# Optimization experiments

Hardware: AMD Instinct MI355X
Metric: run time of the kernel (lower is better)

Reference implementation:

```python
import jax, jax.numpy as jnp
import numpy as np

B, T, V, E, H, C = 64, 512, 32000, 256, 512, 4

def setup_inputs() -> dict:
    key = jax.random.key(0)
    ks = jax.random.split(key, 8)
    s = 1.0 / np.sqrt(H)  # torch LSTM default init scale
    return {
        "x": jax.random.randint(ks[0], (B, T), 0, V),
        "emb": jax.random.normal(ks[1], (V, E), jnp.float32) * 0.1,
        "W_ih": jax.random.uniform(ks[2], (4 * H, E), jnp.float32, -s, s),
        "W_hh": jax.random.uniform(ks[3], (4 * H, H), jnp.float32, -s, s),
        "b_ih": jax.random.uniform(ks[4], (4 * H,), jnp.float32, -s, s),
        "b_hh": jax.random.uniform(ks[5], (4 * H,), jnp.float32, -s, s),
        "W_fc": jax.random.uniform(ks[6], (C, H), jnp.float32, -s, s),
        "b_fc": jax.random.uniform(ks[7], (C,), jnp.float32, -s, s),
    }

def _lstm_last_hidden(e, W_ih, W_hh, b_ih, b_hh):
    # e: [B,T,E]. Precompute input-side gate preactivations for all steps.
    xg = jnp.einsum('bte,ge->tbg', e, W_ih) + (b_ih + b_hh)  # [T,B,4H]
    h0 = jnp.zeros((e.shape[0], H), e.dtype)
    c0 = jnp.zeros((e.shape[0], H), e.dtype)

    def step(carry, xt):
        h, c = carry
        g = xt + h @ W_hh.T                       # [B,4H]
        i, f, gg, o = jnp.split(g, 4, axis=-1)    # torch gate order: i,f,g,o
        i = jax.nn.sigmoid(i)
        f = jax.nn.sigmoid(f)
        gg = jnp.tanh(gg)
        o = jax.nn.sigmoid(o)
        c = f * c + i * gg
        h = o * jnp.tanh(c)
        return (h, c), None

    (hT, _), _ = jax.lax.scan(step, (h0, c0), xg)
    return hT  # last hidden == lstm_out[:, -1, :] for unidirectional LSTM

def reference(x, emb, W_ih, W_hh, b_ih, b_hh, W_fc, b_fc):
    e = emb[x]                                    # [B,T,E] embedding lookup
    hT = _lstm_last_hidden(e, W_ih, W_hh, b_ih, b_hh)
    return hT @ W_fc.T + b_fc                     # [B,C] logits
```

## Files before the change

kernel.cpp:

```cpp
#include <hip/hip_runtime.h>
#include <hip/hip_bf16.h>

#define B_  64
#define T_  512
#define E_  256
#define H_  512
#define G4_ 2048
#define C_  4

typedef __attribute__((ext_vector_type(4))) float  f32x4;
typedef __attribute__((ext_vector_type(8))) __bf16 bf16x8;
typedef __attribute__((ext_vector_type(8))) short  short8;
typedef __attribute__((ext_vector_type(4))) short  s16x4;

union V16 { f32x4 f; bf16x8 b; short8 s; };

__device__ __forceinline__ float sigmoid_(float x) { return 1.0f / (1.0f + __expf(-x)); }
__device__ __forceinline__ float tanh_(float x)    { return 1.0f - 2.0f / (__expf(2.0f * x) + 1.0f); }

__device__ __forceinline__ short f2bf(float f) {
  union { float f; unsigned u; } v; v.f = f;
  return (short)((v.u + 0x7FFFu + ((v.u >> 16) & 1u)) >> 16);
}

__device__ __forceinline__ void store_short_llc(void* p, unsigned v) {
  asm volatile("global_store_short %0, %1, off sc0 sc1" :: "v"(p), "v"(v) : "memory");
}
__device__ __forceinline__ void store_dword_llc(void* p, float v) {
  asm volatile("global_store_dword %0, %1, off sc0 sc1" :: "v"(p), "v"(v) : "memory");
}
__device__ __forceinline__ void load2_dwordx4_llc(const void* p0, const void* p1,
                                                  f32x4* a, f32x4* b) {
  asm volatile(
      "global_load_dwordx4 %0, %2, off sc0 sc1\n\t"
      "global_load_dwordx4 %1, %3, off sc0 sc1\n\t"
      "s_waitcnt vmcnt(0)"
      : "=&v"(*a), "=&v"(*b) : "v"(p0), "v"(p1) : "memory");
}

__global__ __launch_bounds__(256, 1) void wih_conv(const float* __restrict__ W,
                                                   short* __restrict__ out) {
  const int i = (blockIdx.x * 256 + threadIdx.x) * 4;
  f32x4 v = *(const f32x4*)(W + i);
  s16x4 s;
  s[0] = f2bf(v[0]); s[1] = f2bf(v[1]); s[2] = f2bf(v[2]); s[3] = f2bf(v[3]);
  *(s16x4*)(out + i) = s;
}

template<bool WBF16>
__global__ __launch_bounds__(256, 1) void xg_kernel(
    const int* __restrict__ x, const float* __restrict__ emb,
    const void* __restrict__ Wv,
    __hip_bfloat16* __restrict__ xg)
{
  const int t   = blockIdx.x;
  const int tid = threadIdx.x;
  __shared__ int s_idx[B_];
  __shared__ __hip_bfloat16 s_e[B_][E_ + 8];

  if (tid < B_) s_idx[tid] = x[tid * T_ + t];
  __syncthreads();
  {
    int b = tid >> 2, ch = tid & 3;
    const float* src = emb + (size_t)s_idx[b] * E_ + ch * 64;
    short* dst = (short*)&s_e[b][ch * 64];
#pragma unroll
    for (int i = 0; i < 16; i++) {
      f32x4 v = *(const f32x4*)(src + i * 4);
      s16x4 s;
      s[0] = f2bf(v[0]); s[1] = f2bf(v[1]); s[2] = f2bf(v[2]); s[3] = f2bf(v[3]);
      *(s16x4*)(dst + i * 4) = s;
    }
  }
  __syncthreads();

  const int wv   = tid >> 6;
  const int lane = tid & 63;
  const int ln15 = lane & 15, quad = lane >> 4;

  V16 breg[4][8];
#pragma unroll
  for (int nt = 0; nt < 4; nt++)
#pragma unroll
    for (int ks = 0; ks < 8; ks++)
      breg[nt][ks].f = *(const f32x4*)(&s_e[nt * 16 + ln15][quad * 8 + ks * 32]);

  const int gbase = wv * 512;
  const size_t base_t = (size_t)t * (G4_ * B_);
  for (int mt = 0; mt < 32; mt++) {
    const int grow = gbase + mt * 16 + ln15;
    V16 areg[8];
    if constexpr (WBF16) {
      const short* arow = (const short*)Wv + (size_t)grow * E_ + quad * 8;
#pragma unroll
      for (int ks = 0; ks < 8; ks++)
        areg[ks].f = *(const f32x4*)(arow + ks * 32);
    } else {
      const float* arow = (const float*)Wv + (size_t)grow * E_ + quad * 8;
#pragma unroll
      for (int ks = 0; ks < 8; ks++) {
        f32x4 lo = *(const f32x4*)(arow + ks * 32);
        f32x4 hi = *(const f32x4*)(arow + ks * 32 + 4);
        short8 s;
        s[0] = f2bf(lo[0]); s[1] = f2bf(lo[1]); s[2] = f2bf(lo[2]); s[3] = f2bf(lo[3]);
        s[4] = f2bf(hi[0]); s[5] = f2bf(hi[1]); s[6] = f2bf(hi[2]); s[7] = f2bf(hi[3]);
        areg[ks].s = s;
      }
    }

    f32x4 acc[4];
#pragma unroll
    for (int nt = 0; nt < 4; nt++) acc[nt] = (f32x4){0.f, 0.f, 0.f, 0.f};
#pragma unroll
    for (int ks = 0; ks < 8; ks++)
#pragma unroll
      for (int nt = 0; nt < 4; nt++)
        acc[nt] = __builtin_amdgcn_mfma_f32_16x16x32_bf16(areg[ks].b, breg[nt][ks].b, acc[nt], 0, 0, 0);

    const int dbase = mt * 16 + quad * 4;
#pragma unroll
    for (int nt = 0; nt < 4; nt++) {
      const int batch = nt * 16 + ln15;
      s16x4 sv;
#pragma unroll
      for (int r = 0; r < 4; r++) sv[r] = f2bf(acc[nt][r]);
      *(s16x4*)((short*)xg + base_t + ((size_t)wv << 15) + ((size_t)batch << 9) + dbase) = sv;
    }
  }
}

__global__ __launch_bounds__(512, 2) void lstm_kernel(
    const float* __restrict__ W_hh,
    const float* __restrict__ b_ih, const float* __restrict__ b_hh,
    const float* __restrict__ W_fc, const float* __restrict__ b_fc,
    const __hip_bfloat16* __restrict__ xg,
    unsigned int* flags, __hip_bfloat16* hbuf , float* hT,
    float* out)
{
  const int tid  = threadIdx.x;
  const int blk  = blockIdx.x;
  const int pb   = blk & 3;
  const int pd   = blk >> 2;
  const int d0   = pd * 32;
  const int wv   = tid >> 6;
  const int lane = tid & 63;
  const int ln15 = lane & 15, quad = lane >> 4;

  __shared__ __hip_bfloat16 s_h[16][520];
  __shared__ float s_pre[4][16][36];

  V16 areg[16];
  {
    const int grow = (wv >> 1) * 512 + d0 + (wv & 1) * 16 + ln15;
    const float* ap = W_hh + (size_t)grow * H_ + quad * 8;
#pragma unroll
    for (int ks = 0; ks < 16; ks++) {
      f32x4 lo = *(const f32x4*)(ap + ks * 32);
      f32x4 hi = *(const f32x4*)(ap + ks * 32 + 4);
      short8 s;
      s[0] = f2bf(lo[0]); s[1] = f2bf(lo[1]); s[2] = f2bf(lo[2]); s[3] = f2bf(lo[3]);
      s[4] = f2bf(hi[0]); s[5] = f2bf(hi[1]); s[6] = f2bf(hi[2]); s[7] = f2bf(hi[3]);
      areg[ks].s = s;
    }
  }

  const int nb = tid >> 5;
  const int nd = tid & 31;
  const int gb = pb * 16 + nb;
  const int dg = d0 + nd;
  const float bias_i = b_ih[dg]        + b_hh[dg];
  const float bias_f = b_ih[512 + dg]  + b_hh[512 + dg];
  const float bias_g = b_ih[1024 + dg] + b_hh[1024 + dg];
  const float bias_o = b_ih[1536 + dg] + b_hh[1536 + dg];
  float c = 0.0f;
  const int myflag = pb * 16 + pd;

  for (int t = 0; t < T_; t++) {
    const int cur = t & 1, nxt = cur ^ 1;

    const size_t xoff = (size_t)t * (G4_ * B_) + ((size_t)gb << 9) + dg;
    const __hip_bfloat16 xgi = xg[xoff];
    const __hip_bfloat16 xgf = xg[xoff + (1u << 15)];
    const __hip_bfloat16 xgg = xg[xoff + (2u << 15)];
    const __hip_bfloat16 xgo = xg[xoff + (3u << 15)];

    if (tid < 16) {
      const unsigned* fp = flags + pb * 16 + tid;
      while (__hip_atomic_load(fp, __ATOMIC_RELAXED, __HIP_MEMORY_SCOPE_AGENT) < (unsigned)t) {}
    }
    __syncthreads();

    {
      const short* hbase = (const short*)hbuf + (size_t)cur * (B_ * H_) + (size_t)(pb * 16) * H_;
      const int i0 = tid, i1 = tid + 512;
      f32x4 va, vb;
      load2_dwordx4_llc(hbase + i0 * 8, hbase + i1 * 8, &va, &vb);
      *(f32x4*)&s_h[i0 >> 6][(i0 & 63) * 8] = va;
      *(f32x4*)&s_h[i1 >> 6][(i1 & 63) * 8] = vb;
    }
    __syncthreads();

    f32x4 acc0 = (f32x4){0.f, 0.f, 0.f, 0.f};
    f32x4 acc1 = (f32x4){0.f, 0.f, 0.f, 0.f};
#pragma unroll
    for (int ks = 0; ks < 16; ks += 2) {
      V16 b0, b1;
      b0.f = *(const f32x4*)&s_h[ln15][quad * 8 + ks * 32];
      b1.f = *(const f32x4*)&s_h[ln15][quad * 8 + (ks + 1) * 32];
      acc0 = __builtin_amdgcn_mfma_f32_16x16x32_bf16(areg[ks].b,     b0.b, acc0, 0, 0, 0);
      acc1 = __builtin_amdgcn_mfma_f32_16x16x32_bf16(areg[ks + 1].b, b1.b, acc1, 0, 0, 0);
    }
    const f32x4 accs = acc0 + acc1;

    *(f32x4*)&s_pre[wv >> 1][ln15][(wv & 1) * 16 + quad * 4] = accs;
    __syncthreads();

    {
      const float pi = s_pre[0][nb][nd] + bias_i + __bfloat162float(xgi);
      const float pf = s_pre[1][nb][nd] + bias_f + __bfloat162float(xgf);
      const float pg = s_pre[2][nb][nd] + bias_g + __bfloat162float(xgg);
      const float po = s_pre[3][nb][nd] + bias_o + __bfloat162float(xgo);
      const float i_ = sigmoid_(pi), f_ = sigmoid_(pf);
      const float g_ = tanh_(pg),    o_ = sigmoid_(po);
      c = f_ * c + i_ * g_;
      const float h = o_ * tanh_(c);
      if (t < T_ - 1) {
        store_short_llc((short*)hbuf + (size_t)nxt * (B_ * H_) + (size_t)gb * H_ + dg,
                        (unsigned)(unsigned short)f2bf(h));
      } else {
        store_dword_llc(hT + gb * H_ + dg, h);
      }
    }
    __syncthreads();

    if (tid == 0)
      __hip_atomic_store(&flags[myflag], (unsigned)(t + 1),
                         __ATOMIC_RELAXED, __HIP_MEMORY_SCOPE_AGENT);
  }

  if (blk == 0) {
    if (tid < 64)
      while (__hip_atomic_load(&flags[tid], __ATOMIC_RELAXED, __HIP_MEMORY_SCOPE_AGENT) < (unsigned)T_) {}
    __builtin_amdgcn_fence(__ATOMIC_ACQUIRE, "agent");
    __syncthreads();
    for (int o = tid; o < B_ * C_; o += 512) {
      const int b = o >> 2, cl = o & 3;
      const f32x4* hr = (const f32x4*)(hT + b * H_);
      const f32x4* wr = (const f32x4*)(W_fc + cl * H_);
      float s = 0.f;
      for (int d4 = 0; d4 < H_ / 4; d4++) {
        const f32x4 hv = hr[d4];
        const f32x4 wv4 = wr[d4];
        s += hv[0] * wv4[0] + hv[1] * wv4[1] + hv[2] * wv4[2] + hv[3] * wv4[3];
      }
      s += b_fc[cl];
      out[o] = s;
    }
  }
}

extern "C" void kernel_launch(void* const* d_in, const int* in_sizes, int n_in,
                              void* d_out, int out_size, void* d_ws, size_t ws_size,
                              hipStream_t stream) {
  const int*   x    = (const int*)d_in[0];
  const float* emb  = (const float*)d_in[1];
  const float* W_ih = (const float*)d_in[2];
  const float* W_hh = (const float*)d_in[3];
  const float* b_ih = (const float*)d_in[4];
  const float* b_hh = (const float*)d_in[5];
  const float* W_fc = (const float*)d_in[6];
  const float* b_fc = (const float*)d_in[7];
  float* out = (float*)d_out;

  char* ws = (char*)d_ws;
  const size_t XG_OFF  = 524288;
  const size_t XG_END  = XG_OFF + (size_t)T_ * G4_ * B_ * 2;
  const size_t NEEDED2 = XG_END + (size_t)G4_ * E_ * 2;
  if (ws_size < XG_END) return;

  unsigned int*   flags = (unsigned int*)ws;
  __hip_bfloat16* hbuf  = (__hip_bfloat16*)(ws + 4096);
  float*          hT    = (float*)(ws + 135168);
  __hip_bfloat16* xg    = (__hip_bfloat16*)(ws + XG_OFF);
  short*          wih16 = (short*)(ws + XG_END);

  (void)hipMemsetAsync(ws, 0, 135168, stream);

  if (ws_size >= NEEDED2) {
    wih_conv<<<512, 256, 0, stream>>>(W_ih, wih16);
    xg_kernel<true><<<T_, 256, 0, stream>>>(x, emb, wih16, xg);
  } else {
    xg_kernel<false><<<T_, 256, 0, stream>>>(x, emb, W_ih, xg);
  }
  lstm_kernel<<<64, 512, 0, stream>>>(W_hh, b_ih, b_hh, W_fc, b_fc, xg,
                                      flags, hbuf, hT, out);
}
```

Measured before the change: 1.343 ms.

## Repartition LSTM blocks into 8 batch groups by 64 hidden units

The recurrent kernel's 64 blocks are regrouped from 4 batch groups × 32 hidden units into 8 batch groups × 64 hidden units. Each block now waits on only 8 producer flags and reads half as much of h per step, which shrinks the cross-block dependency fan-in. The price is that each wave holds two W_hh tiles and runs two MFMA chains of 16. Because only 8 batches are live, half of each 16-wide MFMA tile is zero padding. That doubles per-step MFMA work and register pressure.

```diff
diff --git a/kernel.cpp b/kernel.cpp
--- a/kernel.cpp
+++ b/kernel.cpp
@@ -29,13 +29,11 @@
 __device__ __forceinline__ void store_dword_llc(void* p, float v) {
   asm volatile("global_store_dword %0, %1, off sc0 sc1" :: "v"(p), "v"(v) : "memory");
 }
-__device__ __forceinline__ void load2_dwordx4_llc(const void* p0, const void* p1,
-                                                  f32x4* a, f32x4* b) {
-  asm volatile(
-      "global_load_dwordx4 %0, %2, off sc0 sc1\n\t"
-      "global_load_dwordx4 %1, %3, off sc0 sc1\n\t"
-      "s_waitcnt vmcnt(0)"
-      : "=&v"(*a), "=&v"(*b) : "v"(p0), "v"(p1) : "memory");
+__device__ __forceinline__ f32x4 ld_b128_llc(const void* p) {
+  f32x4 v;
+  asm volatile("global_load_dwordx4 %0, %1, off sc0 sc1\n\ts_waitcnt vmcnt(0)"
+               : "=&v"(v) : "v"(p) : "memory");
+  return v;
 }
 
 __global__ __launch_bounds__(256, 1) void wih_conv(const float* __restrict__ W,
@@ -139,19 +137,22 @@
 {
   const int tid  = threadIdx.x;
   const int blk  = blockIdx.x;
-  const int pb   = blk & 3;
-  const int pd   = blk >> 2;
-  const int d0   = pd * 32;
+  const int g    = blk & 7;
+  const int pd   = blk >> 3;
+  const int d0   = pd * 64;
   const int wv   = tid >> 6;
   const int lane = tid & 63;
   const int ln15 = lane & 15, quad = lane >> 4;
 
   __shared__ __hip_bfloat16 s_h[16][520];
-  __shared__ float s_pre[4][16][36];
-
-  V16 areg[16];
-  {
-    const int grow = (wv >> 1) * 512 + d0 + (wv & 1) * 16 + ln15;
+  __shared__ float s_pre[4][8][68];
+
+  const int gate  = wv >> 1;
+  const int dhalf = (wv & 1) * 32;
+  V16 areg[2][16];
+#pragma unroll
+  for (int tau = 0; tau < 2; tau++) {
+    const int grow = gate * 512 + d0 + dhalf + tau * 16 + ln15;
     const float* ap = W_hh + (size_t)grow * H_ + quad * 8;
 #pragma unroll
     for (int ks = 0; ks < 16; ks++) {
@@ -160,20 +161,22 @@
       short8 s;
       s[0] = f2bf(lo[0]); s[1] = f2bf(lo[1]); s[2] = f2bf(lo[2]); s[3] = f2bf(lo[3]);
       s[4] = f2bf(hi[0]); s[5] = f2bf(hi[1]); s[6] = f2bf(hi[2]); s[7] = f2bf(hi[3]);
-      areg[ks].s = s;
-    }
-  }
-
-  const int nb = tid >> 5;
-  const int nd = tid & 31;
-  const int gb = pb * 16 + nb;
+      areg[tau][ks].s = s;
+    }
+  }
+
+  const int nb = tid >> 6;
+  const int nd = tid & 63;
+  const int gb = g * 8 + nb;
   const int dg = d0 + nd;
   const float bias_i = b_ih[dg]        + b_hh[dg];
   const float bias_f = b_ih[512 + dg]  + b_hh[512 + dg];
   const float bias_g = b_ih[1024 + dg] + b_hh[1024 + dg];
   const float bias_o = b_ih[1536 + dg] + b_hh[1536 + dg];
   float c = 0.0f;
-  const int myflag = pb * 16 + pd;
+  const int myflag = g * 16 + pd;
+
+  *(f32x4*)&s_h[8 + (tid >> 6)][(tid & 63) * 8] = (f32x4){0.f, 0.f, 0.f, 0.f};
 
   for (int t = 0; t < T_; t++) {
     const int cur = t & 1, nxt = cur ^ 1;
@@ -184,35 +187,33 @@
     const __hip_bfloat16 xgg = xg[xoff + (2u << 15)];
     const __hip_bfloat16 xgo = xg[xoff + (3u << 15)];
 
-    if (tid < 16) {
-      const unsigned* fp = flags + pb * 16 + tid;
+    if (tid < 8) {
+      const unsigned* fp = flags + g * 16 + tid;
       while (__hip_atomic_load(fp, __ATOMIC_RELAXED, __HIP_MEMORY_SCOPE_AGENT) < (unsigned)t) {}
     }
     __syncthreads();
 
     {
-      const short* hbase = (const short*)hbuf + (size_t)cur * (B_ * H_) + (size_t)(pb * 16) * H_;
-      const int i0 = tid, i1 = tid + 512;
-      f32x4 va, vb;
-      load2_dwordx4_llc(hbase + i0 * 8, hbase + i1 * 8, &va, &vb);
-      *(f32x4*)&s_h[i0 >> 6][(i0 & 63) * 8] = va;
-      *(f32x4*)&s_h[i1 >> 6][(i1 & 63) * 8] = vb;
+      const short* hbase = (const short*)hbuf + (size_t)cur * (B_ * H_) + (size_t)(g * 8) * H_;
+      f32x4 va = ld_b128_llc(hbase + tid * 8);
+      *(f32x4*)&s_h[tid >> 6][(tid & 63) * 8] = va;
     }
     __syncthreads();
 
     f32x4 acc0 = (f32x4){0.f, 0.f, 0.f, 0.f};
     f32x4 acc1 = (f32x4){0.f, 0.f, 0.f, 0.f};
 #pragma unroll
-    for (int ks = 0; ks < 16; ks += 2) {
-      V16 b0, b1;
+    for (int ks = 0; ks < 16; ks++) {
+      V16 b0;
       b0.f = *(const f32x4*)&s_h[ln15][quad * 8 + ks * 32];
-      b1.f = *(const f32x4*)&s_h[ln15][quad * 8 + (ks + 1) * 32];
-      acc0 = __builtin_amdgcn_mfma_f32_16x16x32_bf16(areg[ks].b,     b0.b, acc0, 0, 0, 0);
-      acc1 = __builtin_amdgcn_mfma_f32_16x16x32_bf16(areg[ks + 1].b, b1.b, acc1, 0, 0, 0);
-    }
-    const f32x4 accs = acc0 + acc1;
-
-    *(f32x4*)&s_pre[wv >> 1][ln15][(wv & 1) * 16 + quad * 4] = accs;
+      acc0 = __builtin_amdgcn_mfma_f32_16x16x32_bf16(areg[0][ks].b, b0.b, acc0, 0, 0, 0);
+      acc1 = __builtin_amdgcn_mfma_f32_16x16x32_bf16(areg[1][ks].b, b0.b, acc1, 0, 0, 0);
+    }
+
+    if (ln15 < 8) {
+      *(f32x4*)&s_pre[gate][ln15][dhalf + quad * 4]      = acc0;
+      *(f32x4*)&s_pre[gate][ln15][dhalf + 16 + quad * 4] = acc1;
+    }
     __syncthreads();
 
     {
@@ -240,7 +241,8 @@
 
   if (blk == 0) {
     if (tid < 64)
-      while (__hip_atomic_load(&flags[tid], __ATOMIC_RELAXED, __HIP_MEMORY_SCOPE_AGENT) < (unsigned)T_) {}
+      while (__hip_atomic_load(flags + (tid >> 3) * 16 + (tid & 7),
+                               __ATOMIC_RELAXED, __HIP_MEMORY_SCOPE_AGENT) < (unsigned)T_) {}
     __builtin_amdgcn_fence(__ATOMIC_ACQUIRE, "agent");
     __syncthreads();
     for (int o = tid; o < B_ * C_; o += 512) {
```

After: 1.251 ms. 6.8% less time.
